# Kernel optimization log

Measured on AMD Instinct MI355X. Metric: run time of the kernel, lower is better.

Reference implementation:

```python
import jax, jax.numpy as jnp
import numpy as np

B, T, D, H = 4, 2048, 512, 8
DH = D // H
SCALE = DH ** -0.5
CAUSAL = True


def setup_inputs() -> dict:
    key = jax.random.key(0)
    k1, k2, k3, k4 = jax.random.split(key, 4)
    x = jax.random.normal(k1, (B, T, D), dtype=jnp.float32)
    # realistic padding mask: each batch element has a random valid length
    lengths = jax.random.randint(k4, (B,), T // 2, T + 1)
    m = (jnp.arange(T)[None, :] < lengths[:, None]).astype(jnp.float32)[:, :, None]  # (B,T,1)
    w_qkv = jax.random.normal(k2, (D, 3 * D), dtype=jnp.float32) * (D ** -0.5)
    w_out = jax.random.normal(k3, (D, D), dtype=jnp.float32) * (D ** -0.5)
    b_out = jnp.zeros((D,), dtype=jnp.float32)
    return {"x": x, "m": m, "w_qkv": w_qkv, "w_out": w_out, "b_out": b_out}


def reference(x, m, w_qkv, w_out, b_out):
    qkv = x @ w_qkv
    q, k, v = jnp.split(qkv, 3, axis=-1)
    q = q.reshape(B, T, H, DH)
    k = k.reshape(B, T, H, DH)
    v = v.reshape(B, T, H, DH)
    # scores: (b,i,j,h), materialized like the torch module
    e = jnp.einsum('bihd,bjhd->bijh', q, k) * SCALE
    # key-padding mask (b,i,j)
    kpm = m[:, :, None, 0] * m[:, None, :, 0]
    if CAUSAL:
        kpm = jnp.tril(kpm)
    neg = -jnp.finfo(e.dtype).max
    e = jnp.where(kpm[..., None] == 0, neg, e)
    a = jax.nn.softmax(e, axis=2)
    o = jnp.einsum('bijh,bjhd->bihd', a, v).reshape(B, T, D)
    o = o @ w_out + b_out
    return o * m
```

## Files before the change

### kernel.cpp

```cpp
#include <hip/hip_runtime.h>
#include <hip/hip_bf16.h>

#define B_   4
#define T_   2048
#define D_   512
#define H_   8
#define DH_  64
#define BT_  (B_*T_)
#define N3D_ (3*D_)

typedef __bf16  bf16x8 __attribute__((ext_vector_type(8)));
typedef float   f32x4  __attribute__((ext_vector_type(4)));
typedef short   short8 __attribute__((ext_vector_type(8)));
typedef unsigned short u16;

#if defined(__has_builtin)
#if __has_builtin(__builtin_amdgcn_exp2f)
#define EXP2_OK 1
#endif
#endif
#ifndef EXP2_OK
#define EXP2_OK 0
#endif

#if EXP2_OK
#define QSCALE_F (0.125f * 1.44269504088896340736f)
static __device__ __forceinline__ float fastexp(float x) { return __builtin_amdgcn_exp2f(x); }
#else
#define QSCALE_F (0.125f)
static __device__ __forceinline__ float fastexp(float x) { return __expf(x); }
#endif

static __device__ __forceinline__ f32x4 fzero() { f32x4 z = {0.f,0.f,0.f,0.f}; return z; }

static __device__ __forceinline__ f32x4 mfma16(short8 a, short8 b, f32x4 c) {
  return __builtin_amdgcn_mfma_f32_16x16x32_bf16(
      __builtin_bit_cast(bf16x8, a), __builtin_bit_cast(bf16x8, b), c, 0, 0, 0);
}

static __device__ __forceinline__ int swz(int byteoff) {
  return byteoff ^ (((byteoff >> 7) & 7) << 4);
}

static __device__ __forceinline__ u16 bf16bits(float f) {
  __hip_bfloat16 h = __float2bfloat16(f);
  return *reinterpret_cast<u16*>(&h);
}

static __device__ __forceinline__ void gld_lds16(const void* g, void* l) {
  __builtin_amdgcn_global_load_lds(
      (const __attribute__((address_space(1))) void*)g,
      (__attribute__((address_space(3))) void*)l, 16, 0, 0);
}

#define XBLKS 768
__global__ __launch_bounds__(256) void prep_kernel(
    const float* __restrict__ x, const float* __restrict__ wqkv,
    const float* __restrict__ wout,
    u16* __restrict__ xb, u16* __restrict__ wqkvT, u16* __restrict__ woutT) {
  __shared__ u16 lt[64 * 72];
  const int tid = threadIdx.x;
  const int blk = blockIdx.x;

  if (blk < XBLKS) {
    const float4* x4 = reinterpret_cast<const float4*>(x);
    for (int idx = blk * 256 + tid; idx < BT_*D_/8; idx += XBLKS * 256) {
      float4 a = x4[idx*2], b = x4[idx*2+1];
      short8 o;
      o[0] = (short)bf16bits(a.x); o[1] = (short)bf16bits(a.y);
      o[2] = (short)bf16bits(a.z); o[3] = (short)bf16bits(a.w);
      o[4] = (short)bf16bits(b.x); o[5] = (short)bf16bits(b.y);
      o[6] = (short)bf16bits(b.z); o[7] = (short)bf16bits(b.w);
      *reinterpret_cast<short8*>(&xb[idx*8]) = o;
    }
    return;
  }

  int wb = blk - XBLKS;
  const float* src;
  u16* dst;
  int srcld, k0, n0;
  if (wb < 192) {
    src = wqkv; dst = wqkvT; srcld = N3D_;
    k0 = (wb & 7) * 64; n0 = (wb >> 3) * 64;
  } else {
    wb -= 192;
    src = wout; dst = woutT; srcld = D_;
    k0 = (wb & 7) * 64; n0 = (wb >> 3) * 64;
  }
  {
    int c = tid & 63, r0 = tid >> 6;
#pragma unroll
    for (int i = 0; i < 16; ++i) {
      int r = r0 * 16 + i;
      lt[r * 72 + c] = bf16bits(src[(long)(k0 + r) * srcld + n0 + c]);
    }
  }
  __syncthreads();
  {
    int kc = (tid & 7) * 8;
#pragma unroll
    for (int half = 0; half < 2; ++half) {
      int n = (tid >> 3) + half * 32;
      short8 v;
#pragma unroll
      for (int j = 0; j < 8; ++j) v[j] = (short)lt[(kc + j) * 72 + n];
      *reinterpret_cast<short8*>(&dst[(long)(n0 + n) * D_ + k0 + kc]) = v;
    }
  }
}

template <int MODE>
__global__ __launch_bounds__(256) void gemm_kernel(
    const u16* __restrict__ A, const u16* __restrict__ Wt,
    u16* __restrict__ qbuf, u16* __restrict__ kbuf, u16* __restrict__ vtbuf,
    const float* __restrict__ bias, const float* __restrict__ msk,
    float* __restrict__ out) {
  const int NBN = (MODE == 0) ? 12 : 4;
  const int lin = blockIdx.x;
  const int cpx = gridDim.x >> 3;
  const int nn = (lin & 7) * cpx + (lin >> 3);
  const int bm = nn / NBN, bn = nn % NBN;

  const int tid = threadIdx.x;
  const int w = tid >> 6, l = tid & 63;
  const int wr = w >> 1, wc = w & 1;
  const int lr = l & 15, lg = l >> 4;
  const int srow = l >> 3;
  const int scol = ((l & 7) ^ srow) << 4;

  __shared__ char ls[2][32768];

  f32x4 acc[4][4];
#pragma unroll
  for (int i = 0; i < 4; ++i)
#pragma unroll
    for (int j = 0; j < 4; ++j) acc[i][j] = fzero();

  const char* Ab = reinterpret_cast<const char*>(A) + (long)bm * 128 * 1024;
  const char* Wb = reinterpret_cast<const char*>(Wt) + (long)bn * 128 * 1024;

  auto stage = [&](int kt, char* dst) {
#pragma unroll
    for (int c = 0; c < 4; ++c) {
      int chunk = w * 4 + c;
      int row = chunk * 8 + srow;
      gld_lds16(Ab + (long)row * 1024 + kt * 128 + scol, dst + chunk * 1024);
      gld_lds16(Wb + (long)row * 1024 + kt * 128 + scol, dst + 16384 + chunk * 1024);
    }
  };

  stage(0, ls[0]);
  asm volatile("s_waitcnt vmcnt(0)" ::: "memory");
  __builtin_amdgcn_s_barrier();

  int cur = 0;
  for (int kt = 0; kt < 8; ++kt) {
    if (kt + 1 < 8) stage(kt + 1, ls[cur ^ 1]);
    const char* lsA = ls[cur];
    const char* lsB = ls[cur] + 16384;

#pragma unroll
    for (int c = 0; c < 2; ++c) {
      short8 af[4], bfr[4];
#pragma unroll
      for (int mi = 0; mi < 4; ++mi) {
        int row = wr * 64 + mi * 16 + lr;
        af[mi] = *reinterpret_cast<const short8*>(
            lsA + swz(row * 128 + c * 64 + lg * 16));
      }
#pragma unroll
      for (int ni = 0; ni < 4; ++ni) {
        int row = wc * 64 + ni * 16 + lr;
        bfr[ni] = *reinterpret_cast<const short8*>(
            lsB + swz(row * 128 + c * 64 + lg * 16));
      }
      __builtin_amdgcn_s_setprio(1);
#pragma unroll
      for (int mi = 0; mi < 4; ++mi)
#pragma unroll
        for (int ni = 0; ni < 4; ++ni)
          acc[mi][ni] = mfma16(af[mi], bfr[ni], acc[mi][ni]);
      __builtin_amdgcn_s_setprio(0);
    }

    asm volatile("s_waitcnt vmcnt(0)" ::: "memory");
    __builtin_amdgcn_s_barrier();
    cur ^= 1;
  }

  if (MODE == 0) {
    char* lse = &ls[0][0];
    const int which = bn >> 2;
    if (which == 2) {
#pragma unroll
      for (int mi = 0; mi < 4; ++mi)
#pragma unroll
        for (int r = 0; r < 4; ++r) {
          int trow = wr * 64 + mi * 16 + lg * 4 + r;
#pragma unroll
          for (int ni = 0; ni < 4; ++ni) {
            int dcol = wc * 64 + ni * 16 + lr;
            int off = dcol * 256 + trow * 2;
            off ^= ((off >> 8) & 7) << 4;
            *reinterpret_cast<u16*>(lse + off) = bf16bits(acc[mi][ni][r]);
          }
        }
    } else {
      const float scale = (which == 0) ? QSCALE_F : 1.0f;
#pragma unroll
      for (int mi = 0; mi < 4; ++mi)
#pragma unroll
        for (int r = 0; r < 4; ++r) {
          int trow = wr * 64 + mi * 16 + lg * 4 + r;
#pragma unroll
          for (int ni = 0; ni < 4; ++ni) {
            int dcol = wc * 64 + ni * 16 + lr;
            int off = trow * 256 + dcol * 2;
            off ^= ((off >> 8) & 7) << 4;
            *reinterpret_cast<u16*>(lse + off) = bf16bits(acc[mi][ni][r] * scale);
          }
        }
    }
    __syncthreads();
    const int b = bm >> 4;
    const int tb0 = (bm & 15) * 128;
    if (which == 2) {
      const int bn8 = bn - 8;
#pragma unroll
      for (int it = 0; it < 8; ++it) {
        int dp = it * 16 + (tid >> 4);
        int tc = (tid & 15) * 16;
        int off = dp * 256 + (tc ^ ((dp & 7) << 4));
        short8 v = *reinterpret_cast<const short8*>(lse + off);
        int h = 2 * bn8 + (dp >> 6), d = dp & 63;
        long dst = ((long)((b * H_ + h) * DH_ + d)) * T_ + tb0 + tc / 2;
        *reinterpret_cast<short8*>(vtbuf + dst) = v;
      }
    } else {
      u16* obuf = (which == 0) ? qbuf : kbuf;
#pragma unroll
      for (int it = 0; it < 8; ++it) {
        int trow = it * 16 + (tid >> 4);
        int tc = (tid & 15) * 16;
        int off = trow * 256 + (tc ^ ((trow & 7) << 4));
        short8 v = *reinterpret_cast<const short8*>(lse + off);
        int dcol = tc / 2;
        int h = (bn & 3) * 2 + (dcol >> 6), d = dcol & 63;
        long dst = ((long)(b * H_ + h) * T_ + tb0 + trow) * DH_ + d;
        *reinterpret_cast<short8*>(obuf + dst) = v;
      }
    }
  } else {
#pragma unroll
    for (int mi = 0; mi < 4; ++mi) {
#pragma unroll
      for (int r = 0; r < 4; ++r) {
        int grow = bm * 128 + wr * 64 + mi * 16 + lg * 4 + r;
#pragma unroll
        for (int ni = 0; ni < 4; ++ni) {
          int gcol = bn * 128 + wc * 64 + ni * 16 + lr;
          float o = (acc[mi][ni][r] + bias[gcol]) * msk[grow];
          out[(long)grow * D_ + gcol] = o;
        }
      }
    }
  }
}

__global__ __launch_bounds__(512) void attn_kernel(
    const u16* __restrict__ q, const u16* __restrict__ k,
    const u16* __restrict__ vt, const float* __restrict__ msk,
    u16* __restrict__ ao) {
  const int bh = blockIdx.x;
  const int qt = 31 - blockIdx.y;
  const int b = bh >> 3, h = bh & 7;
  const int tid = threadIdx.x;
  const int w = tid >> 6;
  const int wq = w & 3;
  const int hf = w >> 2;
  const int l = tid & 63;
  const int lr = l & 15, lg = l >> 4;

  const float* mrow = msk + b * T_;

  unsigned long long bal = __ballot((l < 32) ? (mrow[l * 64] != 0.f) : false);
  const int nvalid = __popcll(bal);
  if (qt >= nvalid) return;
  const int nkv = (qt + 1 < nvalid) ? (qt + 1) : nvalid;
  const int nh = (nkv - hf + 1) >> 1;
  const int niter = (nkv + 1) >> 1;

  __shared__ char lsK[2 * 2 * 64 * 128];
  __shared__ char lsV[2 * 2 * 64 * 128];
  __shared__ char lsP[8 * 16 * 128];
  char* pbase = lsP + w * (16 * 128);
  char* myK = lsK + hf * 16384;
  char* myV = lsV + hf * 16384;

  const char* kb = reinterpret_cast<const char*>(k)  + (long)bh * T_ * 128;
  const char* vb = reinterpret_cast<const char*>(vt) + (long)bh * DH_ * T_ * 2;
  const char* qb = reinterpret_cast<const char*>(q);

  const int qrow0 = qt * 64 + wq * 16;

  short8 qf[2];
#pragma unroll
  for (int c = 0; c < 2; ++c)
    qf[c] = *reinterpret_cast<const short8*>(
        qb + (((long)bh * T_ + qrow0 + lr) * DH_ + c * 32 + lg * 8) * 2);

  const int srow = l >> 3;
  const int scol = ((l & 7) ^ srow) << 4;

  auto issue = [&](int kt_, int buf) {
#pragma unroll
    for (int c = 0; c < 2; ++c) {
      int chunk = wq * 2 + c;
      int row = chunk * 8 + srow;
      gld_lds16(kb + ((long)kt_ * 64 + row) * 128 + scol,
                myK + buf * 8192 + chunk * 1024);
      gld_lds16(vb + (long)row * (T_ * 2) + kt_ * 128 + scol,
                myV + buf * 8192 + chunk * 1024);
    }
  };

  if (0 < nh) issue(hf, 0);

  float mrun = -__builtin_inff(), lrun = 0.f;
  f32x4 oacc[4];
#pragma unroll
  for (int g = 0; g < 4; ++g) oacc[g] = fzero();

  for (int i = 0; i < niter; ++i) {
    __syncthreads();
    if (i + 1 < nh) issue(2 * (i + 1) + hf, (i + 1) & 1);
    if (i < nh) {
      const int kt = 2 * i + hf;
      const char* lk = myK + (i & 1) * 8192;
      const char* lv = myV + (i & 1) * 8192;

      f32x4 st[4];
      __builtin_amdgcn_s_setprio(1);
#pragma unroll
      for (int ni = 0; ni < 4; ++ni) {
        short8 kf0 = *reinterpret_cast<const short8*>(
            lk + swz((ni * 16 + lr) * 128 + lg * 16));
        short8 kf1 = *reinterpret_cast<const short8*>(
            lk + swz((ni * 16 + lr) * 128 + 64 + lg * 16));
        f32x4 z = fzero();
        z = mfma16(kf0, qf[0], z);
        z = mfma16(kf1, qf[1], z);
        st[ni] = z;
      }
      __builtin_amdgcn_s_setprio(0);

      const bool diag = (kt == qt);
      const bool needcm = (mrow[kt * 64 + 63] == 0.f);
      if (diag || needcm) {
#pragma unroll
        for (int ni = 0; ni < 4; ++ni)
#pragma unroll
          for (int r = 0; r < 4; ++r) {
            int jin = ni * 16 + lg * 4 + r;
            bool bad = (diag && jin > wq * 16 + lr) ||
                       (needcm && mrow[kt * 64 + jin] == 0.f);
            if (bad) st[ni][r] = -3.402823466e38f;
          }
      }

      float pmax = -3.402823466e38f;
#pragma unroll
      for (int ni = 0; ni < 4; ++ni)
#pragma unroll
        for (int r = 0; r < 4; ++r) pmax = fmaxf(pmax, st[ni][r]);
      pmax = fmaxf(pmax, __shfl_xor(pmax, 16));
      pmax = fmaxf(pmax, __shfl_xor(pmax, 32));

      if (!__all(pmax - mrun <= 8.f)) {
        float newm = fmaxf(mrun, pmax);
        float alpha = fastexp(mrun - newm);
        lrun *= alpha;
        mrun = newm;
#pragma unroll
        for (int rr = 0; rr < 4; ++rr) {
          float a = __shfl(alpha, lg * 4 + rr, 16);
#pragma unroll
          for (int g = 0; g < 4; ++g) oacc[g][rr] *= a;
        }
      }

      float p[4][4];
      float rs = 0.f;
#pragma unroll
      for (int ni = 0; ni < 4; ++ni)
#pragma unroll
        for (int r = 0; r < 4; ++r) {
          float pv = fastexp(st[ni][r] - mrun);
          p[ni][r] = pv;
          rs += pv;
        }
      rs += __shfl_xor(rs, 16);
      rs += __shfl_xor(rs, 32);
      lrun += rs;

#pragma unroll
      for (int ni = 0; ni < 4; ++ni)
#pragma unroll
        for (int rp = 0; rp < 2; ++rp) {
          unsigned lo = bf16bits(p[ni][2 * rp]);
          unsigned hi = bf16bits(p[ni][2 * rp + 1]);
          *reinterpret_cast<unsigned*>(
              pbase + swz(lr * 128 + ni * 32 + lg * 8 + rp * 4)) = lo | (hi << 16);
        }
      asm volatile("s_waitcnt lgkmcnt(0)" ::: "memory");

      __builtin_amdgcn_s_setprio(1);
#pragma unroll
      for (int c = 0; c < 2; ++c) {
        short8 pa = *reinterpret_cast<const short8*>(
            pbase + swz(lr * 128 + c * 64 + lg * 16));
#pragma unroll
        for (int g = 0; g < 4; ++g) {
          short8 vf = *reinterpret_cast<const short8*>(
              lv + swz((g * 16 + lr) * 128 + c * 64 + lg * 16));
          oacc[g] = mfma16(pa, vf, oacc[g]);
        }
      }
      __builtin_amdgcn_s_setprio(0);
    }
  }

  __syncthreads();
  float* mO  = reinterpret_cast<float*>(lsK);
  float* mML = reinterpret_cast<float*>(lsK + 4 * 4096);
  if (hf == 1) {
#pragma unroll
    for (int g = 0; g < 4; ++g)
#pragma unroll
      for (int rr = 0; rr < 4; ++rr)
        mO[wq * 1024 + (lg * 4 + rr) * 64 + g * 16 + lr] = oacc[g][rr];
    if (lg == 0) {
      mML[wq * 32 + lr * 2]     = mrun;
      mML[wq * 32 + lr * 2 + 1] = lrun;
    }
  }
  __syncthreads();
  if (hf == 0) {
    float m1 = mML[wq * 32 + lr * 2];
    float l1 = mML[wq * 32 + lr * 2 + 1];
    float M  = fmaxf(mrun, m1);
    float a0 = fastexp(mrun - M);
    float a1 = fastexp(m1 - M);
    float L  = a0 * lrun + a1 * l1;
#pragma unroll
    for (int rr = 0; rr < 4; ++rr) {
      int qrow = lg * 4 + rr;
      float a0r = __shfl(a0, qrow, 16);
      float a1r = __shfl(a1, qrow, 16);
      float Lr  = __shfl(L,  qrow, 16);
      float inv = 1.0f / Lr;
      int t = qrow0 + qrow;
#pragma unroll
      for (int g = 0; g < 4; ++g) {
        float o = a0r * oacc[g][rr] +
                  a1r * mO[wq * 1024 + qrow * 64 + g * 16 + lr];
        ao[((long)(b * T_ + t)) * D_ + h * 64 + g * 16 + lr] = bf16bits(o * inv);
      }
    }
  }
}

extern "C" void kernel_launch(void* const* d_in, const int* in_sizes, int n_in,
                              void* d_out, int out_size, void* d_ws,
                              size_t ws_size, hipStream_t stream) {
  const float* x    = (const float*)d_in[0];
  const float* msk  = (const float*)d_in[1];
  const float* wqkv = (const float*)d_in[2];
  const float* wout = (const float*)d_in[3];
  const float* bout = (const float*)d_in[4];
  float* out = (float*)d_out;

  char* ws = (char*)d_ws;
  u16* xb    = (u16*)(ws);
  u16* wqkvT = (u16*)(ws + 8388608);
  u16* woutT = (u16*)(ws + 9961472);
  u16* qbuf  = (u16*)(ws + 10485760);
  u16* kbuf  = (u16*)(ws + 18874368);
  u16* vtbuf = (u16*)(ws + 27262976);
  u16* ao    = (u16*)(ws + 35651584);

  prep_kernel<<<1024, 256, 0, stream>>>(x, wqkv, wout, xb, wqkvT, woutT);
  gemm_kernel<0><<<(N3D_ / 128) * (BT_ / 128), 256, 0, stream>>>(
      xb, wqkvT, qbuf, kbuf, vtbuf, nullptr, nullptr, nullptr);
  attn_kernel<<<dim3(B_ * H_, T_ / 64), 512, 0, stream>>>(
      qbuf, kbuf, vtbuf, msk, ao);
  gemm_kernel<1><<<(D_ / 128) * (BT_ / 128), 256, 0, stream>>>(
      ao, woutT, nullptr, nullptr, nullptr, bout, msk, out);
}
```

Baseline: 70.68 us.

## Use 256x256-tile 8-wave GEMM with deeper LDS pipeline for QKV projection

Replaces the 128x128-tile QKV projection GEMM with a dedicated 256x256-tile kernel using 512 threads and 128KB of LDS. Its loads run through a finer-grained multi-stage global_load_lds pipeline with explicit vmcnt waits. The larger tile raises arithmetic intensity and cuts operand refetch. The grid shrinks to 192 blocks, which may underfill the 256 CUs, and the high LDS use limits occupancy to one block per CU.

```diff
diff --git a/kernel.cpp b/kernel.cpp
--- a/kernel.cpp
+++ b/kernel.cpp
@@ -51,6 +51,11 @@
   __builtin_amdgcn_global_load_lds(
       (const __attribute__((address_space(1))) void*)g,
       (__attribute__((address_space(3))) void*)l, 16, 0, 0);
+}
+
+template <int N>
+static __device__ __forceinline__ void vwait() {
+  asm volatile("s_waitcnt vmcnt(%0)" :: "i"(N) : "memory");
 }
 
 #define XBLKS 768
@@ -110,13 +115,161 @@
   }
 }
 
-template <int MODE>
+__global__ __launch_bounds__(512) void gemm256_kernel(
+    const u16* __restrict__ A, const u16* __restrict__ Wt,
+    u16* __restrict__ qbuf, u16* __restrict__ kbuf, u16* __restrict__ vtbuf) {
+  const int lin = blockIdx.x;
+  const int cpx = gridDim.x >> 3;
+  const int nn = (lin & 7) * cpx + (lin >> 3);
+  const int bm = nn / 6, bn = nn % 6;
+
+  const int tid = threadIdx.x;
+  const int w = tid >> 6;
+  const int wm = w >> 2, wn = w & 3;
+  const int l = tid & 63;
+  const int lr = l & 15, lg = l >> 4;
+
+  __shared__ char ls[131072];
+
+  f32x4 acc[8][4];
+#pragma unroll
+  for (int i = 0; i < 8; ++i)
+#pragma unroll
+    for (int j = 0; j < 4; ++j) acc[i][j] = fzero();
+
+  const char* Ab = reinterpret_cast<const char*>(A) + (long)bm * 256 * 1024;
+  const char* Wb = reinterpret_cast<const char*>(Wt) + (long)bn * 256 * 1024;
+
+  const int srccol = (l & 3) << 4;
+  const int srow16 = l >> 2;
+  const int colb = lg << 4;
+
+  auto stageHT = [&](int g) {
+    const int ktg = g >> 2, j = g & 3;
+    const char* src = (j & 1) ? Wb : Ab;
+    char* slot = ls + ((ktg & 1) << 16) + (j << 14);
+    const int kcol = ktg * 128 + ((j >> 1) << 6);
+#pragma unroll
+    for (int c = 0; c < 2; ++c) {
+      int chunk = w * 2 + c;
+      int r = chunk * 16 + srow16;
+      gld_lds16(src + (long)r * 1024 + kcol + srccol, slot + chunk * 1024);
+    }
+  };
+
+  stageHT(0); stageHT(1); stageHT(2); stageHT(3); stageHT(4);
+
+  for (int kt = 0; kt < 8; ++kt) {
+    const char* bufb = ls + ((kt & 1) << 16);
+#pragma unroll
+    for (int q = 0; q < 4; ++q) {
+      const int c = q >> 1, mg = q & 1;
+      {
+        int p5 = 4 * kt + q + 5;
+        if (p5 < 32) stageHT(p5);
+      }
+      if (kt == 7) { if (q < 2) vwait<4>(); else vwait<0>(); }
+      else vwait<6>();
+      asm volatile("" ::: "memory");
+      __builtin_amdgcn_s_barrier();
+      asm volatile("" ::: "memory");
+
+      const char* baseA = bufb + ((2 * c) << 14);
+      const char* baseB = bufb + ((2 * c + 1) << 14);
+      short8 af[4], bfr[4];
+#pragma unroll
+      for (int mi = 0; mi < 4; ++mi) {
+        int R = wm * 128 + (mg * 4 + mi) * 16 + lr;
+        af[mi] = *reinterpret_cast<const short8*>(baseA + R * 64 + colb);
+      }
+#pragma unroll
+      for (int ni = 0; ni < 4; ++ni) {
+        int R = wn * 64 + ni * 16 + lr;
+        bfr[ni] = *reinterpret_cast<const short8*>(baseB + R * 64 + colb);
+      }
+      asm volatile("s_waitcnt lgkmcnt(0)" ::: "memory");
+      __builtin_amdgcn_sched_barrier(0);
+      __builtin_amdgcn_s_setprio(1);
+#pragma unroll
+      for (int mi = 0; mi < 4; ++mi)
+#pragma unroll
+        for (int ni = 0; ni < 4; ++ni)
+          acc[mg * 4 + mi][ni] = mfma16(af[mi], bfr[ni], acc[mg * 4 + mi][ni]);
+      __builtin_amdgcn_s_setprio(0);
+    }
+  }
+  asm volatile("" ::: "memory");
+  __builtin_amdgcn_s_barrier();
+  asm volatile("" ::: "memory");
+
+  const int which = bn >> 1;
+  const int b = bm >> 3;
+  const int tb0 = (bm & 7) * 256;
+  if (which == 2) {
+#pragma unroll
+    for (int MI = 0; MI < 8; ++MI)
+#pragma unroll
+      for (int r = 0; r < 4; ++r) {
+        int trow = wm * 128 + MI * 16 + lg * 4 + r;
+#pragma unroll
+        for (int ni = 0; ni < 4; ++ni) {
+          int dcol = wn * 64 + ni * 16 + lr;
+          int off = dcol * 512 + trow * 2;
+          off ^= ((off >> 9) & 7) << 4;
+          *reinterpret_cast<u16*>(ls + off) = bf16bits(acc[MI][ni][r]);
+        }
+      }
+  } else {
+    const float scale = (which == 0) ? QSCALE_F : 1.0f;
+#pragma unroll
+    for (int MI = 0; MI < 8; ++MI)
+#pragma unroll
+      for (int r = 0; r < 4; ++r) {
+        int trow = wm * 128 + MI * 16 + lg * 4 + r;
+#pragma unroll
+        for (int ni = 0; ni < 4; ++ni) {
+          int dcol = wn * 64 + ni * 16 + lr;
+          int off = trow * 512 + dcol * 2;
+          off ^= ((off >> 9) & 7) << 4;
+          *reinterpret_cast<u16*>(ls + off) = bf16bits(acc[MI][ni][r] * scale);
+        }
+      }
+  }
+  __syncthreads();
+  if (which == 2) {
+    const int bnv = bn - 4;
+#pragma unroll
+    for (int it = 0; it < 16; ++it) {
+      int dp = it * 16 + (tid >> 5);
+      int tc = (tid & 31) * 16;
+      int off = (dp * 512 + tc) ^ ((dp & 7) << 4);
+      short8 v = *reinterpret_cast<const short8*>(ls + off);
+      int h = bnv * 4 + (dp >> 6), d = dp & 63;
+      long dst = ((long)((b * H_ + h) * DH_ + d)) * T_ + tb0 + tc / 2;
+      *reinterpret_cast<short8*>(vtbuf + dst) = v;
+    }
+  } else {
+    u16* obuf = (which == 0) ? qbuf : kbuf;
+    const int bq = bn & 1;
+#pragma unroll
+    for (int it = 0; it < 16; ++it) {
+      int trow = it * 16 + (tid >> 5);
+      int tc = (tid & 31) * 16;
+      int off = (trow * 512 + tc) ^ ((trow & 7) << 4);
+      short8 v = *reinterpret_cast<const short8*>(ls + off);
+      int dcol = tc / 2;
+      int h = bq * 4 + (dcol >> 6), d = dcol & 63;
+      long dst = ((long)(b * H_ + h) * T_ + tb0 + trow) * DH_ + d;
+      *reinterpret_cast<short8*>(obuf + dst) = v;
+    }
+  }
+}
+
 __global__ __launch_bounds__(256) void gemm_kernel(
     const u16* __restrict__ A, const u16* __restrict__ Wt,
-    u16* __restrict__ qbuf, u16* __restrict__ kbuf, u16* __restrict__ vtbuf,
     const float* __restrict__ bias, const float* __restrict__ msk,
     float* __restrict__ out) {
-  const int NBN = (MODE == 0) ? 12 : 4;
+  const int NBN = 4;
   const int lin = blockIdx.x;
   const int cpx = gridDim.x >> 3;
   const int nn = (lin & 7) * cpx + (lin >> 3);
@@ -189,80 +342,16 @@
     cur ^= 1;
   }
 
-  if (MODE == 0) {
-    char* lse = &ls[0][0];
-    const int which = bn >> 2;
-    if (which == 2) {
-#pragma unroll
-      for (int mi = 0; mi < 4; ++mi)
-#pragma unroll
-        for (int r = 0; r < 4; ++r) {
-          int trow = wr * 64 + mi * 16 + lg * 4 + r;
-#pragma unroll
-          for (int ni = 0; ni < 4; ++ni) {
-            int dcol = wc * 64 + ni * 16 + lr;
-            int off = dcol * 256 + trow * 2;
-            off ^= ((off >> 8) & 7) << 4;
-            *reinterpret_cast<u16*>(lse + off) = bf16bits(acc[mi][ni][r]);
-          }
-        }
-    } else {
-      const float scale = (which == 0) ? QSCALE_F : 1.0f;
-#pragma unroll
-      for (int mi = 0; mi < 4; ++mi)
-#pragma unroll
-        for (int r = 0; r < 4; ++r) {
-          int trow = wr * 64 + mi * 16 + lg * 4 + r;
-#pragma unroll
-          for (int ni = 0; ni < 4; ++ni) {
-            int dcol = wc * 64 + ni * 16 + lr;
-            int off = trow * 256 + dcol * 2;
-            off ^= ((off >> 8) & 7) << 4;
-            *reinterpret_cast<u16*>(lse + off) = bf16bits(acc[mi][ni][r] * scale);
-          }
-        }
-    }
-    __syncthreads();
-    const int b = bm >> 4;
-    const int tb0 = (bm & 15) * 128;
-    if (which == 2) {
-      const int bn8 = bn - 8;
-#pragma unroll
-      for (int it = 0; it < 8; ++it) {
-        int dp = it * 16 + (tid >> 4);
-        int tc = (tid & 15) * 16;
-        int off = dp * 256 + (tc ^ ((dp & 7) << 4));
-        short8 v = *reinterpret_cast<const short8*>(lse + off);
-        int h = 2 * bn8 + (dp >> 6), d = dp & 63;
-        long dst = ((long)((b * H_ + h) * DH_ + d)) * T_ + tb0 + tc / 2;
-        *reinterpret_cast<short8*>(vtbuf + dst) = v;
-      }
-    } else {
-      u16* obuf = (which == 0) ? qbuf : kbuf;
-#pragma unroll
-      for (int it = 0; it < 8; ++it) {
-        int trow = it * 16 + (tid >> 4);
-        int tc = (tid & 15) * 16;
-        int off = trow * 256 + (tc ^ ((trow & 7) << 4));
-        short8 v = *reinterpret_cast<const short8*>(lse + off);
-        int dcol = tc / 2;
-        int h = (bn & 3) * 2 + (dcol >> 6), d = dcol & 63;
-        long dst = ((long)(b * H_ + h) * T_ + tb0 + trow) * DH_ + d;
-        *reinterpret_cast<short8*>(obuf + dst) = v;
-      }
-    }
-  } else {
-#pragma unroll
-    for (int mi = 0; mi < 4; ++mi) {
-#pragma unroll
-      for (int r = 0; r < 4; ++r) {
-        int grow = bm * 128 + wr * 64 + mi * 16 + lg * 4 + r;
-#pragma unroll
-        for (int ni = 0; ni < 4; ++ni) {
-          int gcol = bn * 128 + wc * 64 + ni * 16 + lr;
-          float o = (acc[mi][ni][r] + bias[gcol]) * msk[grow];
-          out[(long)grow * D_ + gcol] = o;
-        }
+#pragma unroll
+  for (int mi = 0; mi < 4; ++mi) {
+#pragma unroll
+    for (int r = 0; r < 4; ++r) {
+      int grow = bm * 128 + wr * 64 + mi * 16 + lg * 4 + r;
+#pragma unroll
+      for (int ni = 0; ni < 4; ++ni) {
+        int gcol = bn * 128 + wc * 64 + ni * 16 + lr;
+        float o = (acc[mi][ni][r] + bias[gcol]) * msk[grow];
+        out[(long)grow * D_ + gcol] = o;
       }
     }
   }
@@ -491,10 +580,10 @@
   u16* ao    = (u16*)(ws + 35651584);
 
   prep_kernel<<<1024, 256, 0, stream>>>(x, wqkv, wout, xb, wqkvT, woutT);
-  gemm_kernel<0><<<(N3D_ / 128) * (BT_ / 128), 256, 0, stream>>>(
-      xb, wqkvT, qbuf, kbuf, vtbuf, nullptr, nullptr, nullptr);
+  gemm256_kernel<<<(N3D_ / 256) * (BT_ / 256), 512, 0, stream>>>(
+      xb, wqkvT, qbuf, kbuf, vtbuf);
   attn_kernel<<<dim3(B_ * H_, T_ / 64), 512, 0, stream>>>(
       qbuf, kbuf, vtbuf, msk, ao);
-  gemm_kernel<1><<<(D_ / 128) * (BT_ / 128), 256, 0, stream>>>(
-      ao, woutT, nullptr, nullptr, nullptr, bout, msk, out);
-}
+  gemm_kernel<<<(D_ / 128) * (BT_ / 128), 256, 0, stream>>>(
+      ao, woutT, bout, msk, out);
+}
```

Result: slower. 74.98 us (+6.1%).

## Split attention KV loop four ways and give each wave 32 query rows

Applied to the files above, without the earlier changes.

Each attention block now has 2 query-row groups of 32 rows and 4 interleaved KV-tile streams, instead of 4 groups of 16 rows and 2 streams. The aim is to halve the serial KV iteration count per block and reuse each K fragment from LDS across two query subtiles. The final merge now combines four partial softmax states per row through LDS. In exchange, K/V shared memory doubles (about 144KB per block), which likely limits residency to one block per CU. Per-wave register pressure also rises from the doubled accumulators.

```diff
diff --git a/kernel.cpp b/kernel.cpp
--- a/kernel.cpp
+++ b/kernel.cpp
@@ -277,8 +277,8 @@
   const int b = bh >> 3, h = bh & 7;
   const int tid = threadIdx.x;
   const int w = tid >> 6;
-  const int wq = w & 3;
-  const int hf = w >> 2;
+  const int wq2 = w & 1;
+  const int hf = w >> 1;
   const int l = tid & 63;
   const int lr = l & 15, lg = l >> 4;
 
@@ -288,13 +288,13 @@
   const int nvalid = __popcll(bal);
   if (qt >= nvalid) return;
   const int nkv = (qt + 1 < nvalid) ? (qt + 1) : nvalid;
-  const int nh = (nkv - hf + 1) >> 1;
-  const int niter = (nkv + 1) >> 1;
-
-  __shared__ char lsK[2 * 2 * 64 * 128];
-  __shared__ char lsV[2 * 2 * 64 * 128];
-  __shared__ char lsP[8 * 16 * 128];
-  char* pbase = lsP + w * (16 * 128);
+  const int nh = (nkv - hf + 3) >> 2;
+  const int niter = (nkv + 3) >> 2;
+
+  __shared__ char lsK[4 * 2 * 8192];
+  __shared__ char lsV[4 * 2 * 8192];
+  __shared__ char lsP[8 * 2048];
+  char* pbase = lsP + w * 2048;
   char* myK = lsK + hf * 16384;
   char* myV = lsV + hf * 16384;
 
@@ -302,21 +302,23 @@
   const char* vb = reinterpret_cast<const char*>(vt) + (long)bh * DH_ * T_ * 2;
   const char* qb = reinterpret_cast<const char*>(q);
 
-  const int qrow0 = qt * 64 + wq * 16;
-
-  short8 qf[2];
-#pragma unroll
-  for (int c = 0; c < 2; ++c)
-    qf[c] = *reinterpret_cast<const short8*>(
-        qb + (((long)bh * T_ + qrow0 + lr) * DH_ + c * 32 + lg * 8) * 2);
+  short8 qf[2][2];
+#pragma unroll
+  for (int s = 0; s < 2; ++s)
+#pragma unroll
+    for (int c = 0; c < 2; ++c) {
+      int qrow = qt * 64 + wq2 * 32 + s * 16 + lr;
+      qf[s][c] = *reinterpret_cast<const short8*>(
+          qb + (((long)bh * T_ + qrow) * DH_ + c * 32 + lg * 8) * 2);
+    }
 
   const int srow = l >> 3;
   const int scol = ((l & 7) ^ srow) << 4;
 
   auto issue = [&](int kt_, int buf) {
 #pragma unroll
-    for (int c = 0; c < 2; ++c) {
-      int chunk = wq * 2 + c;
+    for (int c = 0; c < 4; ++c) {
+      int chunk = wq2 * 4 + c;
       int row = chunk * 8 + srow;
       gld_lds16(kb + ((long)kt_ * 64 + row) * 128 + scol,
                 myK + buf * 8192 + chunk * 1024);
@@ -327,20 +329,21 @@
 
   if (0 < nh) issue(hf, 0);
 
-  float mrun = -__builtin_inff(), lrun = 0.f;
-  f32x4 oacc[4];
-#pragma unroll
-  for (int g = 0; g < 4; ++g) oacc[g] = fzero();
+  float mrun[2] = {-__builtin_inff(), -__builtin_inff()};
+  float lrun[2] = {0.f, 0.f};
+  f32x4 oaccA[4], oaccB[4];
+#pragma unroll
+  for (int g = 0; g < 4; ++g) { oaccA[g] = fzero(); oaccB[g] = fzero(); }
 
   for (int i = 0; i < niter; ++i) {
     __syncthreads();
-    if (i + 1 < nh) issue(2 * (i + 1) + hf, (i + 1) & 1);
+    if (i + 1 < nh) issue(4 * (i + 1) + hf, (i + 1) & 1);
     if (i < nh) {
-      const int kt = 2 * i + hf;
+      const int kt = 4 * i + hf;
       const char* lk = myK + (i & 1) * 8192;
       const char* lv = myV + (i & 1) * 8192;
 
-      f32x4 st[4];
+      f32x4 st[2][4];
       __builtin_amdgcn_s_setprio(1);
 #pragma unroll
       for (int ni = 0; ni < 4; ++ni) {
@@ -348,10 +351,13 @@
             lk + swz((ni * 16 + lr) * 128 + lg * 16));
         short8 kf1 = *reinterpret_cast<const short8*>(
             lk + swz((ni * 16 + lr) * 128 + 64 + lg * 16));
-        f32x4 z = fzero();
-        z = mfma16(kf0, qf[0], z);
-        z = mfma16(kf1, qf[1], z);
-        st[ni] = z;
+#pragma unroll
+        for (int s = 0; s < 2; ++s) {
+          f32x4 z = fzero();
+          z = mfma16(kf0, qf[s][0], z);
+          z = mfma16(kf1, qf[s][1], z);
+          st[s][ni] = z;
+        }
       }
       __builtin_amdgcn_s_setprio(0);
 
@@ -359,113 +365,142 @@
       const bool needcm = (mrow[kt * 64 + 63] == 0.f);
       if (diag || needcm) {
 #pragma unroll
+        for (int s = 0; s < 2; ++s)
+#pragma unroll
+          for (int ni = 0; ni < 4; ++ni)
+#pragma unroll
+            for (int r = 0; r < 4; ++r) {
+              int jin = ni * 16 + lg * 4 + r;
+              bool bad = (diag && jin > wq2 * 32 + s * 16 + lr) ||
+                         (needcm && mrow[kt * 64 + jin] == 0.f);
+              if (bad) st[s][ni][r] = -3.402823466e38f;
+            }
+      }
+
+#pragma unroll
+      for (int s = 0; s < 2; ++s) {
+        f32x4* oacc = s ? oaccB : oaccA;
+
+        float pmax = -3.402823466e38f;
+#pragma unroll
         for (int ni = 0; ni < 4; ++ni)
 #pragma unroll
+          for (int r = 0; r < 4; ++r) pmax = fmaxf(pmax, st[s][ni][r]);
+        pmax = fmaxf(pmax, __shfl_xor(pmax, 16));
+        pmax = fmaxf(pmax, __shfl_xor(pmax, 32));
+
+        if (!__all(pmax - mrun[s] <= 8.f)) {
+          float newm = fmaxf(mrun[s], pmax);
+          float alpha = fastexp(mrun[s] - newm);
+          lrun[s] *= alpha;
+          mrun[s] = newm;
+#pragma unroll
+          for (int rr = 0; rr < 4; ++rr) {
+            float a = __shfl(alpha, lg * 4 + rr, 16);
+#pragma unroll
+            for (int g = 0; g < 4; ++g) oacc[g][rr] *= a;
+          }
+        }
+
+        float p[4][4];
+        float rs = 0.f;
+#pragma unroll
+        for (int ni = 0; ni < 4; ++ni)
+#pragma unroll
           for (int r = 0; r < 4; ++r) {
-            int jin = ni * 16 + lg * 4 + r;
-            bool bad = (diag && jin > wq * 16 + lr) ||
-                       (needcm && mrow[kt * 64 + jin] == 0.f);
-            if (bad) st[ni][r] = -3.402823466e38f;
+            float pv = fastexp(st[s][ni][r] - mrun[s]);
+            p[ni][r] = pv;
+            rs += pv;
           }
-      }
-
-      float pmax = -3.402823466e38f;
-#pragma unroll
-      for (int ni = 0; ni < 4; ++ni)
-#pragma unroll
-        for (int r = 0; r < 4; ++r) pmax = fmaxf(pmax, st[ni][r]);
-      pmax = fmaxf(pmax, __shfl_xor(pmax, 16));
-      pmax = fmaxf(pmax, __shfl_xor(pmax, 32));
-
-      if (!__all(pmax - mrun <= 8.f)) {
-        float newm = fmaxf(mrun, pmax);
-        float alpha = fastexp(mrun - newm);
-        lrun *= alpha;
-        mrun = newm;
-#pragma unroll
-        for (int rr = 0; rr < 4; ++rr) {
-          float a = __shfl(alpha, lg * 4 + rr, 16);
-#pragma unroll
-          for (int g = 0; g < 4; ++g) oacc[g][rr] *= a;
-        }
-      }
-
-      float p[4][4];
-      float rs = 0.f;
-#pragma unroll
-      for (int ni = 0; ni < 4; ++ni)
-#pragma unroll
-        for (int r = 0; r < 4; ++r) {
-          float pv = fastexp(st[ni][r] - mrun);
-          p[ni][r] = pv;
-          rs += pv;
-        }
-      rs += __shfl_xor(rs, 16);
-      rs += __shfl_xor(rs, 32);
-      lrun += rs;
-
-#pragma unroll
-      for (int ni = 0; ni < 4; ++ni)
-#pragma unroll
-        for (int rp = 0; rp < 2; ++rp) {
-          unsigned lo = bf16bits(p[ni][2 * rp]);
-          unsigned hi = bf16bits(p[ni][2 * rp + 1]);
-          *reinterpret_cast<unsigned*>(
-              pbase + swz(lr * 128 + ni * 32 + lg * 8 + rp * 4)) = lo | (hi << 16);
-        }
-      asm volatile("s_waitcnt lgkmcnt(0)" ::: "memory");
-
-      __builtin_amdgcn_s_setprio(1);
-#pragma unroll
-      for (int c = 0; c < 2; ++c) {
-        short8 pa = *reinterpret_cast<const short8*>(
-            pbase + swz(lr * 128 + c * 64 + lg * 16));
-#pragma unroll
-        for (int g = 0; g < 4; ++g) {
-          short8 vf = *reinterpret_cast<const short8*>(
-              lv + swz((g * 16 + lr) * 128 + c * 64 + lg * 16));
-          oacc[g] = mfma16(pa, vf, oacc[g]);
-        }
-      }
-      __builtin_amdgcn_s_setprio(0);
+        rs += __shfl_xor(rs, 16);
+        rs += __shfl_xor(rs, 32);
+        lrun[s] += rs;
+
+#pragma unroll
+        for (int ni = 0; ni < 4; ++ni)
+#pragma unroll
+          for (int rp = 0; rp < 2; ++rp) {
+            unsigned lo = bf16bits(p[ni][2 * rp]);
+            unsigned hi = bf16bits(p[ni][2 * rp + 1]);
+            *reinterpret_cast<unsigned*>(
+                pbase + swz(lr * 128 + ni * 32 + lg * 8 + rp * 4)) =
+                lo | (hi << 16);
+          }
+        asm volatile("s_waitcnt lgkmcnt(0)" ::: "memory");
+
+        __builtin_amdgcn_s_setprio(1);
+#pragma unroll
+        for (int c = 0; c < 2; ++c) {
+          short8 pa = *reinterpret_cast<const short8*>(
+              pbase + swz(lr * 128 + c * 64 + lg * 16));
+#pragma unroll
+          for (int g = 0; g < 4; ++g) {
+            short8 vf = *reinterpret_cast<const short8*>(
+                lv + swz((g * 16 + lr) * 128 + c * 64 + lg * 16));
+            oacc[g] = mfma16(pa, vf, oacc[g]);
+          }
+        }
+        __builtin_amdgcn_s_setprio(0);
+      }
     }
   }
 
   __syncthreads();
   float* mO  = reinterpret_cast<float*>(lsK);
-  float* mML = reinterpret_cast<float*>(lsK + 4 * 4096);
-  if (hf == 1) {
-#pragma unroll
-    for (int g = 0; g < 4; ++g)
-#pragma unroll
-      for (int rr = 0; rr < 4; ++rr)
-        mO[wq * 1024 + (lg * 4 + rr) * 64 + g * 16 + lr] = oacc[g][rr];
-    if (lg == 0) {
-      mML[wq * 32 + lr * 2]     = mrun;
-      mML[wq * 32 + lr * 2 + 1] = lrun;
+  float* mML = reinterpret_cast<float*>(lsV);
+  if (hf != 0) {
+    const int hb = wq2 * 3 + (hf - 1);
+#pragma unroll
+    for (int s = 0; s < 2; ++s) {
+      const f32x4* oacc = s ? oaccB : oaccA;
+      int base = (hb * 2 + s) * 1024;
+#pragma unroll
+      for (int g = 0; g < 4; ++g)
+#pragma unroll
+        for (int rr = 0; rr < 4; ++rr)
+          mO[base + (lg * 4 + rr) * 64 + g * 16 + lr] = oacc[g][rr];
+      if (lg == 0) {
+        mML[(hb * 2 + s) * 32 + lr * 2]     = mrun[s];
+        mML[(hb * 2 + s) * 32 + lr * 2 + 1] = lrun[s];
+      }
     }
   }
   __syncthreads();
   if (hf == 0) {
-    float m1 = mML[wq * 32 + lr * 2];
-    float l1 = mML[wq * 32 + lr * 2 + 1];
-    float M  = fmaxf(mrun, m1);
-    float a0 = fastexp(mrun - M);
-    float a1 = fastexp(m1 - M);
-    float L  = a0 * lrun + a1 * l1;
-#pragma unroll
-    for (int rr = 0; rr < 4; ++rr) {
-      int qrow = lg * 4 + rr;
-      float a0r = __shfl(a0, qrow, 16);
-      float a1r = __shfl(a1, qrow, 16);
-      float Lr  = __shfl(L,  qrow, 16);
-      float inv = 1.0f / Lr;
-      int t = qrow0 + qrow;
-#pragma unroll
-      for (int g = 0; g < 4; ++g) {
-        float o = a0r * oacc[g][rr] +
-                  a1r * mO[wq * 1024 + qrow * 64 + g * 16 + lr];
-        ao[((long)(b * T_ + t)) * D_ + h * 64 + g * 16 + lr] = bf16bits(o * inv);
+#pragma unroll
+    for (int s = 0; s < 2; ++s) {
+      const f32x4* oacc = s ? oaccB : oaccA;
+      float m1 = mML[((wq2 * 3 + 0) * 2 + s) * 32 + lr * 2];
+      float l1 = mML[((wq2 * 3 + 0) * 2 + s) * 32 + lr * 2 + 1];
+      float m2 = mML[((wq2 * 3 + 1) * 2 + s) * 32 + lr * 2];
+      float l2 = mML[((wq2 * 3 + 1) * 2 + s) * 32 + lr * 2 + 1];
+      float m3 = mML[((wq2 * 3 + 2) * 2 + s) * 32 + lr * 2];
+      float l3 = mML[((wq2 * 3 + 2) * 2 + s) * 32 + lr * 2 + 1];
+      float M = fmaxf(fmaxf(mrun[s], m1), fmaxf(m2, m3));
+      float a0 = fastexp(mrun[s] - M);
+      float a1 = fastexp(m1 - M);
+      float a2 = fastexp(m2 - M);
+      float a3 = fastexp(m3 - M);
+      float L = a0 * lrun[s] + a1 * l1 + a2 * l2 + a3 * l3;
+#pragma unroll
+      for (int rr = 0; rr < 4; ++rr) {
+        int qrow = lg * 4 + rr;
+        float a0r = __shfl(a0, qrow, 16);
+        float a1r = __shfl(a1, qrow, 16);
+        float a2r = __shfl(a2, qrow, 16);
+        float a3r = __shfl(a3, qrow, 16);
+        float Lr  = __shfl(L,  qrow, 16);
+        float inv = 1.0f / Lr;
+        int t = qt * 64 + wq2 * 32 + s * 16 + qrow;
+#pragma unroll
+        for (int g = 0; g < 4; ++g) {
+          float o = a0r * oacc[g][rr] +
+                    a1r * mO[((wq2 * 3 + 0) * 2 + s) * 1024 + qrow * 64 + g * 16 + lr] +
+                    a2r * mO[((wq2 * 3 + 1) * 2 + s) * 1024 + qrow * 64 + g * 16 + lr] +
+                    a3r * mO[((wq2 * 3 + 2) * 2 + s) * 1024 + qrow * 64 + g * 16 + lr];
+          ao[((long)(b * T_ + t)) * D_ + h * 64 + g * 16 + lr] =
+              bf16bits(o * inv);
+        }
       }
     }
   }
```

Result: slower. 93.85 us (+32.8%).
